# Optimization experiments

Hardware: AMD Instinct MI355X
Metric: run time of the kernel (lower is better)

The kernel has to match this reference:

```python
import jax, jax.numpy as jnp
import numpy as np

N = 100000
E = 1600000
D_IN = 128
D_HID = 128
D_OUT = 128


def setup_inputs() -> dict:
    key = jax.random.key(0)
    k1, k2, k3, k4 = jax.random.split(key, 4)
    x_piece = jax.random.normal(k1, (N, D_IN), dtype=jnp.float32)
    edge_index_piece = jax.random.randint(k2, (2, E), 0, N, dtype=jnp.int64)
    # GCNConv parameters (Glorot-ish scale)
    W1 = jax.random.normal(k3, (D_IN, D_HID), dtype=jnp.float32) / np.sqrt(D_IN)
    b1 = jnp.zeros((D_HID,), dtype=jnp.float32)
    W2 = jax.random.normal(k4, (D_HID, D_OUT), dtype=jnp.float32) / np.sqrt(D_HID)
    b2 = jnp.zeros((D_OUT,), dtype=jnp.float32)
    return {"x_piece": x_piece, "edge_index_piece": edge_index_piece,
            "W1": W1, "b1": b1, "W2": W2, "b2": b2}


def gcn_conv(x, W, b, src, dst, n):
    """PyG GCNConv: out = D^-1/2 (A+I) D^-1/2 (x W) + b, with self-loops."""
    # x: [n, d_in], W: [d_in, d_out], src/dst: [E+n] (self-loops included)
    h = x @ W  # [n, d_out]
    deg = jax.ops.segment_sum(jnp.ones_like(dst, dtype=h.dtype), dst, num_segments=n)
    dinv = jnp.where(deg > 0, jax.lax.rsqrt(deg), 0.0)  # deg^-1/2
    norm = dinv[src] * dinv[dst]  # [E+n]
    msg = h[src] * norm[:, None]  # gather + normalize
    agg = jax.ops.segment_sum(msg, dst, num_segments=n)  # scatter-add
    return agg + b


def reference(x_piece, edge_index_piece, W1, b1, W2, b2):
    n = x_piece.shape[0]
    loops = jnp.arange(n, dtype=edge_index_piece.dtype)
    src = jnp.concatenate([edge_index_piece[0], loops])
    dst = jnp.concatenate([edge_index_piece[1], loops])
    h = gcn_conv(x_piece, W1, b1, src, dst, n)
    h = jax.nn.relu(h)
    out = gcn_conv(h, W2, b2, src, dst, n)
    return out
```

## Files before the change

kernel.cpp:

```cpp
#include <hip/hip_runtime.h>
#include <hip/hip_bf16.h>


#define D 128
#define BUKBITS 7
#define BUKSZ 128
#define MAXBUK 1024
#define SCHUNK 16384

typedef __attribute__((ext_vector_type(8))) short short8;
typedef __attribute__((ext_vector_type(4))) float f32x4;

static __device__ __forceinline__ ushort f2b(float f) {
    __hip_bfloat16 h = __float2bfloat16(f);
    return *reinterpret_cast<ushort*>(&h);
}


__global__ __launch_bounds__(256) void k_bukhist(const int* __restrict__ dst, int* __restrict__ bukcnt,
                                                 int E, int nbuk) {
    __shared__ int lh[MAXBUK];
    for (int i = threadIdx.x; i < nbuk; i += 256) lh[i] = 0;
    __syncthreads();
    int start = blockIdx.x * SCHUNK;
    int end = min(E, start + SCHUNK);
    for (int e = start + threadIdx.x; e < end; e += 256)
        atomicAdd(&lh[dst[e] >> BUKBITS], 1);
    __syncthreads();
    for (int i = threadIdx.x; i < nbuk; i += 256)
        if (lh[i]) atomicAdd(&bukcnt[i], lh[i]);
}

__global__ __launch_bounds__(256) void k_bukscan(const int* __restrict__ bukcnt, int* __restrict__ bukbase,
                                                 int* __restrict__ gcur, int nbuk, int E) {
    __shared__ int vals[MAXBUK];
    __shared__ int tsum[256];
    int t = threadIdx.x;
    for (int i = t; i < MAXBUK; i += 256) vals[i] = (i < nbuk) ? bukcnt[i] : 0;
    __syncthreads();
    int o = t * 4;
    int s = vals[o] + vals[o + 1] + vals[o + 2] + vals[o + 3];
    tsum[t] = s;
    __syncthreads();
    for (int off = 1; off < 256; off <<= 1) {
        int v = (t >= off) ? tsum[t - off] : 0;
        __syncthreads();
        tsum[t] += v;
        __syncthreads();
    }
    int run = tsum[t] - s;
    for (int i = 0; i < 4; i++) {
        int idx = o + i;
        if (idx < nbuk) { bukbase[idx] = run; gcur[idx] = run; }
        run += vals[idx];
    }
    if (t == 0) bukbase[nbuk] = E;
}

__global__ __launch_bounds__(256) void k_scatter(const int* __restrict__ src, const int* __restrict__ dst,
                                                 int* __restrict__ gcur, uint* __restrict__ tmp,
                                                 int E, int nbuk) {
    __shared__ int lh[MAXBUK];
    __shared__ int lbase[MAXBUK];
    for (int i = threadIdx.x; i < nbuk; i += 256) lh[i] = 0;
    __syncthreads();
    int start = blockIdx.x * SCHUNK;
    int end = min(E, start + SCHUNK);
    for (int e = start + threadIdx.x; e < end; e += 256)
        atomicAdd(&lh[dst[e] >> BUKBITS], 1);
    __syncthreads();
    for (int i = threadIdx.x; i < nbuk; i += 256) {
        int c = lh[i];
        lbase[i] = c ? atomicAdd(&gcur[i], c) : 0;
        lh[i] = 0;
    }
    __syncthreads();
    for (int e = start + threadIdx.x; e < end; e += 256) {
        int s = src[e];
        int d = dst[e];
        int bk = d >> BUKBITS;
        int r = atomicAdd(&lh[bk], 1);
        tmp[lbase[bk] + r] = ((uint)(d & (BUKSZ - 1)) << 25) | (uint)s;
    }
}

__global__ __launch_bounds__(256) void k_fillC(const uint* __restrict__ tmp, const int* __restrict__ bukbase,
                                               int* __restrict__ eord, int* __restrict__ rowptr,
                                               float* __restrict__ dinv, int n, int nbuk) {
    __shared__ int cnt[BUKSZ];
    __shared__ int sc[BUKSZ];
    __shared__ int lrp[BUKSZ];
    int b = blockIdx.x;
    int node0 = b << BUKBITS;
    int nn = min(BUKSZ, n - node0);
    int e0 = bukbase[b], e1 = bukbase[b + 1];
    int t = threadIdx.x;
    if (t < BUKSZ) cnt[t] = 0;
    __syncthreads();
    for (int e = e0 + t; e < e1; e += 256)
        atomicAdd(&cnt[tmp[e] >> 25], 1);
    __syncthreads();
    int c0 = (t < BUKSZ) ? cnt[t] : 0;
    if (t < BUKSZ) sc[t] = c0;
    __syncthreads();
    for (int off = 1; off < BUKSZ; off <<= 1) {
        int v = (t < BUKSZ && t >= off) ? sc[t - off] : 0;
        __syncthreads();
        if (t < BUKSZ) sc[t] += v;
        __syncthreads();
    }
    if (t < BUKSZ) lrp[t] = e0 + sc[t] - c0;
    if (t < nn) {
        rowptr[node0 + t] = e0 + sc[t] - c0;
        dinv[node0 + t] = 1.0f / sqrtf((float)(c0 + 1));
    }
    if (b == nbuk - 1 && t == 0) rowptr[n] = e1;
    __syncthreads();
    if (t < BUKSZ) cnt[t] = 0;
    __syncthreads();
    for (int e = e0 + t; e < e1; e += 256) {
        uint u = tmp[e];
        int dL = (int)(u >> 25);
        int s = (int)(u & 0x1FFFFFFu);
        int r = atomicAdd(&cnt[dL], 1);
        eord[lrp[dL] + r] = s;
    }
}

__global__ __launch_bounds__(256) void k_prepW(const float* __restrict__ W1, const float* __restrict__ W2,
                                               ushort* __restrict__ Wt1, ushort* __restrict__ Wt2) {
    int i = blockIdx.x * 256 + threadIdx.x;
    if (i < 16384) {
        int kk = i >> 7, nn = i & 127;
        Wt1[nn * 128 + kk] = f2b(W1[i]);
        Wt2[nn * 128 + kk] = f2b(W2[i]);
    }
}

template <bool ABF16>
__global__ __launch_bounds__(256) void k_gemm(const void* __restrict__ Xv, const ushort* __restrict__ Wt,
                                              const float* __restrict__ dinv, ushort* __restrict__ Hb,
                                              int nrows) {
    const int wave = threadIdx.x >> 6;
    const int lane = threadIdx.x & 63;
    const int quad = lane >> 4;
    const int m = lane & 15;
    const int row0 = blockIdx.x * 64 + wave * 16;
    const int rowc = min(row0 + m, nrows - 1);

    f32x4 acc[8];
    #pragma unroll
    for (int t = 0; t < 8; t++) acc[t] = (f32x4){0.f, 0.f, 0.f, 0.f};

    #pragma unroll
    for (int ks = 0; ks < 4; ks++) {
        const int k0 = ks * 32 + quad * 8;
        short8 a;
        if (ABF16) {
            a = *(const short8*)((const ushort*)Xv + (size_t)rowc * D + k0);
        } else {
            const float* p = (const float*)Xv + (size_t)rowc * D + k0;
            float4 u0 = ((const float4*)p)[0];
            float4 u1 = ((const float4*)p)[1];
            a[0] = (short)f2b(u0.x); a[1] = (short)f2b(u0.y);
            a[2] = (short)f2b(u0.z); a[3] = (short)f2b(u0.w);
            a[4] = (short)f2b(u1.x); a[5] = (short)f2b(u1.y);
            a[6] = (short)f2b(u1.z); a[7] = (short)f2b(u1.w);
        }
        #pragma unroll
        for (int t = 0; t < 8; t++) {
            short8 b = *(const short8*)(Wt + ((t * 16 + m) * D + k0));
            acc[t] = __builtin_amdgcn_mfma_f32_16x16x32_bf16(a, b, acc[t], 0, 0, 0);
        }
    }
    #pragma unroll
    for (int r = 0; r < 4; r++) {
        int orow = row0 + quad * 4 + r;
        if (orow < nrows) {
            float dvv = dinv[orow];
            #pragma unroll
            for (int t = 0; t < 8; t++)
                Hb[(size_t)orow * D + t * 16 + m] = f2b(acc[t][r] * dvv);
        }
    }
}

template <bool RELU, bool OBF16>
__global__ __launch_bounds__(256) void k_agg(const ushort* __restrict__ Hb, const float* __restrict__ dinv,
                                             const int* __restrict__ rowptr, const int* __restrict__ eord,
                                             const float* __restrict__ bias, void* __restrict__ outp, int n) {
    int v = blockIdx.x * 4 + (threadIdx.x >> 6);
    int lane = threadIdx.x & 63;
    if (v >= n) return;
    float dv = dinv[v];
    const uint* __restrict__ Hu = (const uint*)Hb;
    uint hs = Hu[(size_t)v * 64 + lane];
    float ax = __uint_as_float(hs << 16);
    float ay = __uint_as_float(hs & 0xffff0000u);
    int e = rowptr[v];
    const int end = rowptr[v + 1];
    for (; e + 15 < end; e += 16) {
        int s[16];
        #pragma unroll
        for (int i = 0; i < 16; i++) s[i] = eord[e + i];
        uint h[16];
        #pragma unroll
        for (int i = 0; i < 16; i++) h[i] = Hu[(size_t)s[i] * 64 + lane];
        #pragma unroll
        for (int i = 0; i < 16; i++) {
            ax += __uint_as_float(h[i] << 16);
            ay += __uint_as_float(h[i] & 0xffff0000u);
        }
    }
    for (; e + 3 < end; e += 4) {
        int s[4];
        #pragma unroll
        for (int i = 0; i < 4; i++) s[i] = eord[e + i];
        uint h[4];
        #pragma unroll
        for (int i = 0; i < 4; i++) h[i] = Hu[(size_t)s[i] * 64 + lane];
        #pragma unroll
        for (int i = 0; i < 4; i++) {
            ax += __uint_as_float(h[i] << 16);
            ay += __uint_as_float(h[i] & 0xffff0000u);
        }
    }
    for (; e < end; ++e) {
        uint hh = Hu[(size_t)eord[e] * 64 + lane];
        ax += __uint_as_float(hh << 16);
        ay += __uint_as_float(hh & 0xffff0000u);
    }
    float2 bb = ((const float2*)bias)[lane];
    float rx = dv * ax + bb.x;
    float ry = dv * ay + bb.y;
    if (RELU) { rx = fmaxf(rx, 0.f); ry = fmaxf(ry, 0.f); }
    if (OBF16) {
        uint w = ((uint)f2b(ry) << 16) | (uint)f2b(rx);
        ((uint*)outp)[(size_t)v * 64 + lane] = w;
    } else {
        ((float2*)((float*)outp + (size_t)v * D))[lane] = make_float2(rx, ry);
    }
}


static inline size_t alignup(size_t x) { return (x + 511) & ~(size_t)511; }

extern "C" void kernel_launch(void* const* d_in, const int* in_sizes, int n_in,
                              void* d_out, int out_size, void* d_ws, size_t ws_size,
                              hipStream_t stream) {
    const float* x  = (const float*)d_in[0];
    const int* eidx = (const int*)d_in[1];
    const float* W1 = (const float*)d_in[2];
    const float* b1 = (const float*)d_in[3];
    const float* W2 = (const float*)d_in[4];
    const float* b2 = (const float*)d_in[5];
    float* out = (float*)d_out;

    const int N = in_sizes[0] / D;
    const int E = in_sizes[1] / 2;
    const int* src = eidx;
    const int* dst = eidx + E;
    const int nbuk = (N + BUKSZ - 1) >> BUKBITS;

    char* ws = (char*)d_ws;
    size_t off = 0;
    int* bukcnt = (int*)(ws + off);   off = alignup(off + (size_t)MAXBUK * 4);
    int* bukbase = (int*)(ws + off);  off = alignup(off + (size_t)(MAXBUK + 1) * 4);
    int* gcur   = (int*)(ws + off);   off = alignup(off + (size_t)MAXBUK * 4);
    int* rowptr = (int*)(ws + off);   off = alignup(off + (size_t)(N + 1) * 4);
    float* dinv = (float*)(ws + off); off = alignup(off + (size_t)N * 4);
    int* eord   = (int*)(ws + off);   off = alignup(off + (size_t)E * 4);
    ushort* hbuf = (ushort*)(ws + off); off = alignup(off + (size_t)N * D * 2);
    ushort* act  = (ushort*)(ws + off); off = alignup(off + (size_t)N * D * 2);
    ushort* Wt1 = (ushort*)(ws + off); off = alignup(off + 16384 * 2);
    ushort* Wt2 = (ushort*)(ws + off); off = alignup(off + 16384 * 2);
    uint* tmp = (uint*)hbuf;
    (void)ws_size;

    const int nT = 256;
    const int gChunk = (E + SCHUNK - 1) / SCHUNK;

    hipMemsetAsync(bukcnt, 0, (size_t)MAXBUK * 4, stream);
    k_prepW<<<64, nT, 0, stream>>>(W1, W2, Wt1, Wt2);
    k_bukhist<<<gChunk, nT, 0, stream>>>(dst, bukcnt, E, nbuk);
    k_bukscan<<<1, nT, 0, stream>>>(bukcnt, bukbase, gcur, nbuk, E);
    k_scatter<<<gChunk, nT, 0, stream>>>(src, dst, gcur, tmp, E, nbuk);
    k_fillC<<<nbuk, nT, 0, stream>>>(tmp, bukbase, eord, rowptr, dinv, N, nbuk);

    const int gGemm = (N + 63) / 64;
    const int gAgg = (N + 3) / 4;

    k_gemm<false><<<gGemm, nT, 0, stream>>>((const void*)x, Wt1, dinv, hbuf, N);
    k_agg<true, true><<<gAgg, nT, 0, stream>>>(hbuf, dinv, rowptr, eord, b1, (void*)act, N);

    k_gemm<true><<<gGemm, nT, 0, stream>>>((const void*)act, Wt2, dinv, hbuf, N);
    k_agg<false, false><<<gAgg, nT, 0, stream>>>(hbuf, dinv, rowptr, eord, b2, (void*)out, N);
}
```

Measured before the change: 368.8 us.

## Slice aggregation by feature columns across blocks with persistent grid-stride waves

The aggregation kernel is restructured so that the 128 feature columns are split into 8 slices of 32 bytes, with the slice chosen by the block index. Within a wave, 8 edges are gathered at once, each by a group of 8 lanes, and the partial sums are combined with cross-lane shuffles. A fixed persistent grid of 2048 blocks walks the nodes with a grid-stride loop. The aim is to keep each slice's working set of the gathered bf16 features small enough to get more L2/MALL reuse, and to raise memory-level parallelism. In exchange, each row's edge indices are now read once per slice (8 times in total), only 8 lanes write output, and the shuffle reduction adds work.

Result: slower. 694.9 us (+88.4%).

```diff
diff --git a/kernel.cpp b/kernel.cpp
--- a/kernel.cpp
+++ b/kernel.cpp
@@ -7,6 +7,10 @@
 #define BUKSZ 128
 #define MAXBUK 1024
 #define SCHUNK 16384
+
+#define NSLICE 8
+#define AGG_BLOCKS 2048
+#define WAVES_PER_SLICE 1024
 
 typedef __attribute__((ext_vector_type(8))) short short8;
 typedef __attribute__((ext_vector_type(4))) float f32x4;
@@ -186,59 +190,61 @@
 }
 
 template <bool RELU, bool OBF16>
-__global__ __launch_bounds__(256) void k_agg(const ushort* __restrict__ Hb, const float* __restrict__ dinv,
-                                             const int* __restrict__ rowptr, const int* __restrict__ eord,
-                                             const float* __restrict__ bias, void* __restrict__ outp, int n) {
-    int v = blockIdx.x * 4 + (threadIdx.x >> 6);
-    int lane = threadIdx.x & 63;
-    if (v >= n) return;
-    float dv = dinv[v];
+__global__ __launch_bounds__(256, 8) void k_agg_slice(const ushort* __restrict__ Hb,
+                                                      const float* __restrict__ dinv,
+                                                      const int* __restrict__ rowptr,
+                                                      const int* __restrict__ eord,
+                                                      const float* __restrict__ bias,
+                                                      void* __restrict__ outp, int n) {
+    const int slice = blockIdx.x & (NSLICE - 1);
+    const int blk = blockIdx.x >> 3;
+    const int wid = (blk << 2) + (threadIdx.x >> 6);
+    const int lane = threadIdx.x & 63;
+    const int g = lane >> 3;
+    const int w = lane & 7;
+    const int cofs = slice * 8 + w;
     const uint* __restrict__ Hu = (const uint*)Hb;
-    uint hs = Hu[(size_t)v * 64 + lane];
-    float ax = __uint_as_float(hs << 16);
-    float ay = __uint_as_float(hs & 0xffff0000u);
-    int e = rowptr[v];
-    const int end = rowptr[v + 1];
-    for (; e + 15 < end; e += 16) {
-        int s[16];
-        #pragma unroll
-        for (int i = 0; i < 16; i++) s[i] = eord[e + i];
-        uint h[16];
-        #pragma unroll
-        for (int i = 0; i < 16; i++) h[i] = Hu[(size_t)s[i] * 64 + lane];
-        #pragma unroll
-        for (int i = 0; i < 16; i++) {
-            ax += __uint_as_float(h[i] << 16);
-            ay += __uint_as_float(h[i] & 0xffff0000u);
-        }
-    }
-    for (; e + 3 < end; e += 4) {
-        int s[4];
-        #pragma unroll
-        for (int i = 0; i < 4; i++) s[i] = eord[e + i];
-        uint h[4];
-        #pragma unroll
-        for (int i = 0; i < 4; i++) h[i] = Hu[(size_t)s[i] * 64 + lane];
-        #pragma unroll
-        for (int i = 0; i < 4; i++) {
-            ax += __uint_as_float(h[i] << 16);
-            ay += __uint_as_float(h[i] & 0xffff0000u);
-        }
-    }
-    for (; e < end; ++e) {
-        uint hh = Hu[(size_t)eord[e] * 64 + lane];
-        ax += __uint_as_float(hh << 16);
-        ay += __uint_as_float(hh & 0xffff0000u);
-    }
-    float2 bb = ((const float2*)bias)[lane];
-    float rx = dv * ax + bb.x;
-    float ry = dv * ay + bb.y;
-    if (RELU) { rx = fmaxf(rx, 0.f); ry = fmaxf(ry, 0.f); }
-    if (OBF16) {
-        uint w = ((uint)f2b(ry) << 16) | (uint)f2b(rx);
-        ((uint*)outp)[(size_t)v * 64 + lane] = w;
-    } else {
-        ((float2*)((float*)outp + (size_t)v * D))[lane] = make_float2(rx, ry);
+    const float2 bb = ((const float2*)bias)[cofs];
+
+    for (int v = wid; v < n; v += WAVES_PER_SLICE) {
+        float ax = 0.f, ay = 0.f;
+        int e = rowptr[v];
+        const int end = rowptr[v + 1];
+        for (; e + 15 < end; e += 16) {
+            int s0 = eord[e + g];
+            int s1 = eord[e + 8 + g];
+            uint h0 = Hu[(size_t)s0 * 64 + cofs];
+            uint h1 = Hu[(size_t)s1 * 64 + cofs];
+            ax += __uint_as_float(h0 << 16) + __uint_as_float(h1 << 16);
+            ay += __uint_as_float(h0 & 0xffff0000u) + __uint_as_float(h1 & 0xffff0000u);
+        }
+        for (; e + 7 < end; e += 8) {
+            int s0 = eord[e + g];
+            uint h0 = Hu[(size_t)s0 * 64 + cofs];
+            ax += __uint_as_float(h0 << 16);
+            ay += __uint_as_float(h0 & 0xffff0000u);
+        }
+        if (e + g < end) {
+            int s0 = eord[e + g];
+            uint h0 = Hu[(size_t)s0 * 64 + cofs];
+            ax += __uint_as_float(h0 << 16);
+            ay += __uint_as_float(h0 & 0xffff0000u);
+        }
+        ax += __shfl_xor(ax, 8);  ay += __shfl_xor(ay, 8);
+        ax += __shfl_xor(ax, 16); ay += __shfl_xor(ay, 16);
+        ax += __shfl_xor(ax, 32); ay += __shfl_xor(ay, 32);
+        if (lane < 8) {
+            uint hs = Hu[(size_t)v * 64 + cofs];
+            float dv = dinv[v];
+            float rx = dv * (ax + __uint_as_float(hs << 16)) + bb.x;
+            float ry = dv * (ay + __uint_as_float(hs & 0xffff0000u)) + bb.y;
+            if (RELU) { rx = fmaxf(rx, 0.f); ry = fmaxf(ry, 0.f); }
+            if (OBF16) {
+                ((uint*)outp)[(size_t)v * 64 + cofs] = ((uint)f2b(ry) << 16) | (uint)f2b(rx);
+            } else {
+                ((float2*)outp)[(size_t)v * 64 + cofs] = make_float2(rx, ry);
+            }
+        }
     }
 }
 
@@ -288,11 +294,10 @@
     k_fillC<<<nbuk, nT, 0, stream>>>(tmp, bukbase, eord, rowptr, dinv, N, nbuk);
 
     const int gGemm = (N + 63) / 64;
-    const int gAgg = (N + 3) / 4;
 
     k_gemm<false><<<gGemm, nT, 0, stream>>>((const void*)x, Wt1, dinv, hbuf, N);
-    k_agg<true, true><<<gAgg, nT, 0, stream>>>(hbuf, dinv, rowptr, eord, b1, (void*)act, N);
+    k_agg_slice<true, true><<<AGG_BLOCKS, nT, 0, stream>>>(hbuf, dinv, rowptr, eord, b1, (void*)act, N);
 
     k_gemm<true><<<gGemm, nT, 0, stream>>>((const void*)act, Wt2, dinv, hbuf, N);
-    k_agg<false, false><<<gAgg, nT, 0, stream>>>(hbuf, dinv, rowptr, eord, b2, (void*)out, N);
-}
+    k_agg_slice<false, false><<<AGG_BLOCKS, nT, 0, stream>>>(hbuf, dinv, rowptr, eord, b2, (void*)out, N);
+}
```
